# Optimization experiments

Measured on AMD Instinct MI355X. Metric: run time of the kernel, lower is better.

The kernel has to match this reference:

```python
import jax, jax.numpy as jnp
import numpy as np

B, N = 32, 2048
NUM_FEATURE, NUM_CLUSTER, D_MODEL = 512, 256, 1024
LN_EPS = 1e-5
NEG_SLOPE = 0.2


def setup_inputs() -> dict:
    key = jax.random.key(0)
    ks = jax.random.split(key, 8)
    s_feat = 1.0 / np.sqrt(NUM_FEATURE)
    s_city = 1.0 / np.sqrt(NUM_CLUSTER)
    return {
        "input": jax.random.normal(ks[0], (B, N, NUM_FEATURE), dtype=jnp.float32),
        "static": jax.random.normal(ks[1], (N, NUM_CLUSTER), dtype=jnp.float32),
        # torch.nn.Linear stores weight as [out, in]
        "W_feat": jax.random.uniform(ks[2], (D_MODEL, NUM_FEATURE), jnp.float32, -s_feat, s_feat),
        "b_feat": jax.random.uniform(ks[3], (D_MODEL,), jnp.float32, -s_feat, s_feat),
        "W_city": jax.random.uniform(ks[4], (D_MODEL, NUM_CLUSTER), jnp.float32, -s_city, s_city),
        "b_city": jax.random.uniform(ks[5], (D_MODEL,), jnp.float32, -s_city, s_city),
        "gamma": jnp.ones((D_MODEL,), dtype=jnp.float32),
        "beta": jnp.zeros((D_MODEL,), dtype=jnp.float32),
    }


def reference(input, static, W_feat, b_feat, W_city, b_city, gamma, beta):
    # x = leaky_relu(feat_embed(input), 0.2)  -> [B, N, d_model]
    x = jnp.einsum("bnf,df->bnd", input, W_feat) + b_feat
    x = jnp.where(x >= 0, x, NEG_SLOPE * x)
    # c = city_embed(static) -> [N, d_model]; diag_embed + matmul == elementwise gate
    c = jnp.einsum("nk,dk->nd", static, W_city) + b_city
    x = x * c[None, :, :]
    # LayerNorm over d_model (eps=1e-5, elementwise affine)
    mu = jnp.mean(x, axis=-1, keepdims=True)
    var = jnp.mean(jnp.square(x - mu), axis=-1, keepdims=True)
    x = (x - mu) * jax.lax.rsqrt(var + LN_EPS)
    return x * gamma + beta
```

## Files before the change

### kernel.cpp

```cpp
#include <hip/hip_runtime.h>
#include <hip/hip_bf16.h>


typedef __attribute__((ext_vector_type(8))) short short8;
typedef __attribute__((ext_vector_type(4))) float f32x4;

__device__ __forceinline__ unsigned short f2bf(float f) {
    unsigned int u = __float_as_uint(f);
    return (unsigned short)((u + 0x7FFFu + ((u >> 16) & 1u)) >> 16);
}
__device__ __forceinline__ float b2f(unsigned short h) {
    return __uint_as_float(((unsigned int)h) << 16);
}

#define LDS_ASYNC16(g, l) __builtin_amdgcn_global_load_lds(                 \
    (const __attribute__((address_space(1))) void*)(g),                     \
    (__attribute__((address_space(3))) void*)(l), 16, 0, 0)

__global__ __launch_bounds__(256) void convw_kernel(
    const float* __restrict__ w, unsigned short* __restrict__ o)
{
    int i = (blockIdx.x * 256 + threadIdx.x) * 4;
    float4 v = *(const float4*)(w + i);
    uint2 p;
    p.x = (unsigned)f2bf(v.x) | ((unsigned)f2bf(v.y) << 16);
    p.y = (unsigned)f2bf(v.z) | ((unsigned)f2bf(v.w) << 16);
    *(uint2*)(o + i) = p;
}

__global__ __launch_bounds__(256) void city_kernel(
    const float* __restrict__ st,
    const float* __restrict__ Wc,
    const float* __restrict__ bc,
    unsigned short* __restrict__ cg)
{
    __shared__ __align__(16) unsigned short Sa[64 * 264];
    __shared__ __align__(16) unsigned short Sb[128 * 264];
    const int t  = threadIdx.x;
    const int n0 = blockIdx.x << 6;
    const int d0 = blockIdx.y << 7;

    #pragma unroll
    for (int i = 0; i < 16; ++i) {
        int idx = (i << 8) + t;
        int row = idx >> 6, kq = (idx & 63) << 2;
        float4 v = *(const float4*)(st + (size_t)(n0 + row) * 256 + kq);
        uint2 p;
        p.x = (unsigned)f2bf(v.x) | ((unsigned)f2bf(v.y) << 16);
        p.y = (unsigned)f2bf(v.z) | ((unsigned)f2bf(v.w) << 16);
        *(uint2*)(Sa + row * 264 + kq) = p;
    }
    #pragma unroll
    for (int i = 0; i < 32; ++i) {
        int idx = (i << 8) + t;
        int row = idx >> 6, kq = (idx & 63) << 2;
        float4 v = *(const float4*)(Wc + (size_t)(d0 + row) * 256 + kq);
        uint2 p;
        p.x = (unsigned)f2bf(v.x) | ((unsigned)f2bf(v.y) << 16);
        p.y = (unsigned)f2bf(v.z) | ((unsigned)f2bf(v.w) << 16);
        *(uint2*)(Sb + row * 264 + kq) = p;
    }
    __syncthreads();

    const int wv = t >> 6;
    const int cl = t & 15, q = (t >> 4) & 3;
    f32x4 acc[4][2];
    #pragma unroll
    for (int rt = 0; rt < 4; ++rt)
        #pragma unroll
        for (int ct = 0; ct < 2; ++ct) acc[rt][ct] = (f32x4)0.f;

    #pragma unroll
    for (int ks = 0; ks < 8; ++ks) {
        short8 a[4];
        #pragma unroll
        for (int rt = 0; rt < 4; ++rt)
            a[rt] = *(const short8*)(Sa + ((rt << 4) + cl) * 264 + (ks << 5) + (q << 3));
        #pragma unroll
        for (int ct = 0; ct < 2; ++ct) {
            short8 bf8 = *(const short8*)(Sb + ((wv << 5) + (ct << 4) + cl) * 264 + (ks << 5) + (q << 3));
            #pragma unroll
            for (int rt = 0; rt < 4; ++rt)
                acc[rt][ct] = __builtin_amdgcn_mfma_f32_16x16x32_bf16(a[rt], bf8, acc[rt][ct], 0, 0, 0);
        }
    }
    #pragma unroll
    for (int ct = 0; ct < 2; ++ct) {
        const int d = d0 + (wv << 5) + (ct << 4) + cl;
        const float bcv = bc[d];
        #pragma unroll
        for (int rt = 0; rt < 4; ++rt)
            #pragma unroll
            for (int rr = 0; rr < 4; ++rr) {
                const int row = (rt << 4) + (q << 2) + rr;
                cg[(size_t)(n0 + row) * 1024 + d] = f2bf(acc[rt][ct][rr] + bcv);
            }
    }
}

__global__ __launch_bounds__(512, 2) void feat_kernel(
    const float* __restrict__ inp,
    const unsigned short* __restrict__ Wf,
    const float* __restrict__ b_feat,
    const unsigned short* __restrict__ cg,
    const float* __restrict__ gamma,
    const float* __restrict__ beta,
    float* __restrict__ out)
{
    __shared__ __align__(16) unsigned short Bs[2][32768];
    __shared__ __align__(16) unsigned short As[2][2560];

    const int t    = threadIdx.x;
    const int lane = t & 63;
    const int w    = t >> 6;
    const int cl   = lane & 15;
    const int q    = lane >> 4;
    const int m0   = blockIdx.x << 6;
    const int n0   = m0 & 2047;

    f32x4 acc[4][8];
    #pragma unroll
    for (int rt = 0; rt < 4; ++rt)
        #pragma unroll
        for (int ct = 0; ct < 8; ++ct) acc[rt][ct] = (f32x4)0.f;

    const int arow = t >> 3, akq = (t & 7) << 2;
    const float* ap = inp + (size_t)(m0 + arow) * 512 + akq;

    const unsigned short* bgp = Wf + (size_t)((w << 4) + cl) * 512 + (q << 3);

    #pragma unroll
    for (int i = 0; i < 8; ++i)
        LDS_ASYNC16(bgp + ((size_t)i << 16), &Bs[0][(w << 9) + (i << 12)]);
    {
        float4 av = *(const float4*)ap;
        uint2 p;
        p.x = (unsigned)f2bf(av.x) | ((unsigned)f2bf(av.y) << 16);
        p.y = (unsigned)f2bf(av.z) | ((unsigned)f2bf(av.w) << 16);
        *(uint2*)(&As[0][arow * 40 + akq]) = p;
    }
    __syncthreads();

    for (int kb = 0; kb < 16; ++kb) {
        const int b = kb & 1;
        float4 av;
        if (kb < 15) {
            const int k0n = (kb + 1) << 5;
            #pragma unroll
            for (int i = 0; i < 8; ++i)
                LDS_ASYNC16(bgp + k0n + ((size_t)i << 16), &Bs[b ^ 1][(w << 9) + (i << 12)]);
            av = *(const float4*)(ap + k0n);
        }
        short8 a[4];
        #pragma unroll
        for (int rt = 0; rt < 4; ++rt)
            a[rt] = *(const short8*)(&As[b][((rt << 4) + cl) * 40 + (q << 3)]);
        #pragma unroll
        for (int ct = 0; ct < 8; ++ct) {
            short8 bf8 = *(const short8*)(&Bs[b][(((w << 3) + ct) << 9) + (q << 7) + (cl << 3)]);
            #pragma unroll
            for (int rt = 0; rt < 4; ++rt)
                acc[rt][ct] = __builtin_amdgcn_mfma_f32_16x16x32_bf16(a[rt], bf8, acc[rt][ct], 0, 0, 0);
        }
        if (kb < 15) {
            uint2 p;
            p.x = (unsigned)f2bf(av.x) | ((unsigned)f2bf(av.y) << 16);
            p.y = (unsigned)f2bf(av.z) | ((unsigned)f2bf(av.w) << 16);
            *(uint2*)(&As[b ^ 1][arow * 40 + akq]) = p;
        }
        __syncthreads();
    }

    float* red1 = (float*)&As[0][0];
    float* red2 = red1 + 512;
    float* smu  = red1 + 1024;
    float* srs  = red1 + 1088;

    float bfv[8];
    #pragma unroll
    for (int ct = 0; ct < 8; ++ct) bfv[ct] = b_feat[(w << 7) + (ct << 4) + cl];

    #pragma unroll
    for (int rt = 0; rt < 4; ++rt) {
        #pragma unroll
        for (int rr = 0; rr < 4; ++rr) {
            const int row = (rt << 4) + (q << 2) + rr;
            float s1 = 0.f, s2 = 0.f;
            #pragma unroll
            for (int ct = 0; ct < 8; ++ct) {
                const int d = (w << 7) + (ct << 4) + cl;
                float x = acc[rt][ct][rr] + bfv[ct];
                x = (x >= 0.f) ? x : 0.2f * x;
                x *= b2f(cg[(size_t)(n0 + row) * 1024 + d]);
                acc[rt][ct][rr] = x;
                s1 += x;
                s2 += x * x;
            }
            #pragma unroll
            for (int off = 1; off < 16; off <<= 1) {
                s1 += __shfl_xor(s1, off, 64);
                s2 += __shfl_xor(s2, off, 64);
            }
            if (cl == 0) {
                red1[(w << 6) + row] = s1;
                red2[(w << 6) + row] = s2;
            }
        }
    }
    __syncthreads();
    if (t < 64) {
        float a = 0.f, bb = 0.f;
        #pragma unroll
        for (int j = 0; j < 8; ++j) { a += red1[(j << 6) + t]; bb += red2[(j << 6) + t]; }
        const float mu  = a * (1.0f / 1024.0f);
        const float var = bb * (1.0f / 1024.0f) - mu * mu;
        smu[t] = mu;
        srs[t] = rsqrtf(var + 1e-5f);
    }
    __syncthreads();

    #pragma unroll
    for (int ct = 0; ct < 8; ++ct) {
        const int d = (w << 7) + (ct << 4) + cl;
        const float g = gamma[d], be = beta[d];
        #pragma unroll
        for (int rt = 0; rt < 4; ++rt) {
            #pragma unroll
            for (int rr = 0; rr < 4; ++rr) {
                const int row = (rt << 4) + (q << 2) + rr;
                out[(size_t)(m0 + row) * 1024 + d] =
                    (acc[rt][ct][rr] - smu[row]) * srs[row] * g + be;
            }
        }
    }
}

extern "C" void kernel_launch(void* const* d_in, const int* in_sizes, int n_in,
                              void* d_out, int out_size, void* d_ws, size_t ws_size,
                              hipStream_t stream) {
    const float* inp   = (const float*)d_in[0];
    const float* st    = (const float*)d_in[1];
    const float* Wf    = (const float*)d_in[2];
    const float* bfeat = (const float*)d_in[3];
    const float* Wc    = (const float*)d_in[4];
    const float* bc    = (const float*)d_in[5];
    const float* gamma = (const float*)d_in[6];
    const float* beta  = (const float*)d_in[7];
    float* out = (float*)d_out;

    unsigned short* wsWf = (unsigned short*)d_ws;
    unsigned short* wsC  = (unsigned short*)((char*)d_ws + (1 << 20));

    convw_kernel<<<512, 256, 0, stream>>>(Wf, wsWf);
    city_kernel<<<dim3(32, 8), 256, 0, stream>>>(st, Wc, bc, wsC);
    feat_kernel<<<1024, 512, 0, stream>>>(inp, wsWf, bfeat, wsC, gamma, beta, out);
}
```

Measured before the change: 582.1 us.

## Drop LDS staging in feat GEMM; load MFMA operands directly from global

The feat kernel no longer stages A and B tiles through double-buffered shared memory with async global-to-LDS copies and per-iteration barriers. Each lane now loads its MFMA fragments straight from global memory and converts fp32 input to bf16 with the packed v_cvt_pk_bf16_f32 instruction. The K loop is fully unrolled and shared memory shrinks to the LayerNorm reduction buffers. This removes barrier and LDS traffic and may raise occupancy, but every wave now reads the same weight and input data separately, with strided, less coalesced accesses that rely on cache reuse.

```diff
diff --git a/kernel.cpp b/kernel.cpp
--- a/kernel.cpp
+++ b/kernel.cpp
@@ -12,10 +12,6 @@
 __device__ __forceinline__ float b2f(unsigned short h) {
     return __uint_as_float(((unsigned int)h) << 16);
 }
-
-#define LDS_ASYNC16(g, l) __builtin_amdgcn_global_load_lds(                 \
-    (const __attribute__((address_space(1))) void*)(g),                     \
-    (__attribute__((address_space(3))) void*)(l), 16, 0, 0)
 
 __global__ __launch_bounds__(256) void convw_kernel(
     const float* __restrict__ w, unsigned short* __restrict__ o)
@@ -107,8 +103,10 @@
     const float* __restrict__ beta,
     float* __restrict__ out)
 {
-    __shared__ __align__(16) unsigned short Bs[2][32768];
-    __shared__ __align__(16) unsigned short As[2][2560];
+    __shared__ float red1[512];
+    __shared__ float red2[512];
+    __shared__ float smu[64];
+    __shared__ float srs[64];
 
     const int t    = threadIdx.x;
     const int lane = t & 63;
@@ -124,57 +122,35 @@
         #pragma unroll
         for (int ct = 0; ct < 8; ++ct) acc[rt][ct] = (f32x4)0.f;
 
-    const int arow = t >> 3, akq = (t & 7) << 2;
-    const float* ap = inp + (size_t)(m0 + arow) * 512 + akq;
-
-    const unsigned short* bgp = Wf + (size_t)((w << 4) + cl) * 512 + (q << 3);
-
-    #pragma unroll
-    for (int i = 0; i < 8; ++i)
-        LDS_ASYNC16(bgp + ((size_t)i << 16), &Bs[0][(w << 9) + (i << 12)]);
-    {
-        float4 av = *(const float4*)ap;
-        uint2 p;
-        p.x = (unsigned)f2bf(av.x) | ((unsigned)f2bf(av.y) << 16);
-        p.y = (unsigned)f2bf(av.z) | ((unsigned)f2bf(av.w) << 16);
-        *(uint2*)(&As[0][arow * 40 + akq]) = p;
-    }
-    __syncthreads();
-
+    const float* ap = inp + (size_t)(m0 + cl) * 512 + (q << 3);
+    const unsigned short* bp = Wf + (size_t)((w << 7) + cl) * 512 + (q << 3);
+
+    #pragma unroll
     for (int kb = 0; kb < 16; ++kb) {
-        const int b = kb & 1;
-        float4 av;
-        if (kb < 15) {
-            const int k0n = (kb + 1) << 5;
-            #pragma unroll
-            for (int i = 0; i < 8; ++i)
-                LDS_ASYNC16(bgp + k0n + ((size_t)i << 16), &Bs[b ^ 1][(w << 9) + (i << 12)]);
-            av = *(const float4*)(ap + k0n);
-        }
+        const int k0 = kb << 5;
         short8 a[4];
         #pragma unroll
-        for (int rt = 0; rt < 4; ++rt)
-            a[rt] = *(const short8*)(&As[b][((rt << 4) + cl) * 40 + (q << 3)]);
+        for (int rt = 0; rt < 4; ++rt) {
+            const float* r = ap + (size_t)(rt << 4) * 512 + k0;
+            float4 lo = *(const float4*)(r);
+            float4 hi = *(const float4*)(r + 4);
+            unsigned p0, p1, p2, p3;
+            asm("v_cvt_pk_bf16_f32 %0, %1, %2" : "=v"(p0) : "v"(lo.x), "v"(lo.y));
+            asm("v_cvt_pk_bf16_f32 %0, %1, %2" : "=v"(p1) : "v"(lo.z), "v"(lo.w));
+            asm("v_cvt_pk_bf16_f32 %0, %1, %2" : "=v"(p2) : "v"(hi.x), "v"(hi.y));
+            asm("v_cvt_pk_bf16_f32 %0, %1, %2" : "=v"(p3) : "v"(hi.z), "v"(hi.w));
+            union { unsigned u[4]; short8 s; } cv;
+            cv.u[0] = p0; cv.u[1] = p1; cv.u[2] = p2; cv.u[3] = p3;
+            a[rt] = cv.s;
+        }
         #pragma unroll
         for (int ct = 0; ct < 8; ++ct) {
-            short8 bf8 = *(const short8*)(&Bs[b][(((w << 3) + ct) << 9) + (q << 7) + (cl << 3)]);
+            short8 bf8 = *(const short8*)(bp + (size_t)(ct << 4) * 512 + k0);
             #pragma unroll
             for (int rt = 0; rt < 4; ++rt)
                 acc[rt][ct] = __builtin_amdgcn_mfma_f32_16x16x32_bf16(a[rt], bf8, acc[rt][ct], 0, 0, 0);
         }
-        if (kb < 15) {
-            uint2 p;
-            p.x = (unsigned)f2bf(av.x) | ((unsigned)f2bf(av.y) << 16);
-            p.y = (unsigned)f2bf(av.z) | ((unsigned)f2bf(av.w) << 16);
-            *(uint2*)(&As[b ^ 1][arow * 40 + akq]) = p;
-        }
-        __syncthreads();
-    }
-
-    float* red1 = (float*)&As[0][0];
-    float* red2 = red1 + 512;
-    float* smu  = red1 + 1024;
-    float* srs  = red1 + 1088;
+    }
 
     float bfv[8];
     #pragma unroll
```

After: 620.1 us. +6.5%, slower.
